# Performance work log

Hardware: AMD Instinct MI355X
Metric: run time of the kernel (lower is better)

## Reference

```python
import jax, jax.numpy as jnp
import numpy as np

CHN = 64
C8 = CHN // 8          # 8
ANG_IN = 5
ANG_OUT = 5
BU, V, H, W = 8, ANG_IN, 64, 64


def setup_inputs() -> dict:
    key = jax.random.key(0)
    ks = jax.random.split(key, 7)
    s = 0.05
    buffer = jax.random.normal(ks[0], (BU, CHN, V, H, W), jnp.float32)
    # 1x1x1 Conv3d weights stored as [out_ch, in_ch]
    Wq = jax.random.normal(ks[1], (C8, CHN), jnp.float32) * s
    Wk = jax.random.normal(ks[2], (C8, CHN), jnp.float32) * s
    Wv = jax.random.normal(ks[3], (C8 * ANG_OUT, CHN), jnp.float32) * s
    Wc = jax.random.normal(ks[4], (C8 * ANG_OUT, CHN), jnp.float32) * s
    # out block: Conv3d(40->64, k=(1,1,7), pad (0,0,3)); Conv3d(64->64, k=(7,1,1), pad (3,0,0))
    W1 = jax.random.normal(ks[5], (CHN, C8 * ANG_IN, 1, 1, 7), jnp.float32) * s
    W2 = jax.random.normal(ks[6], (CHN, CHN, 7, 1, 1), jnp.float32) * s
    return {"buffer": buffer, "Wq": Wq, "Wk": Wk, "Wv": Wv, "Wc": Wc, "W1": W1, "W2": W2}


def _pointwise(Wo, x):
    # 1x1x1 Conv3d == channel GEMM
    return jnp.einsum('oc,bcvhw->bovhw', Wo, x)


def reference(buffer, Wq, Wk, Wv, Wc, W1, W2):
    bu, c, v, h, w = buffer.shape
    q = _pointwise(Wq, buffer)      # [bu, c8, v, h, w]
    k = _pointwise(Wk, buffer)      # [bu, c8, v, h, w]
    val = _pointwise(Wv, buffer)    # [bu, c8*ar_out, v, h, w]

    def flat(x):  # 'bu c v h w -> bu c h (v w)'
        return x.transpose(0, 1, 3, 2, 4).reshape(bu, x.shape[1], h, v * w)

    qf, kf, vf = flat(q), flat(k), flat(val)
    attn = jax.nn.softmax(jnp.einsum('bchm,bchn->bhmn', qf, kf), axis=-1)  # [bu,h,vw,vw]
    out = jnp.einsum('bhmn,bchn->bchm', attn, vf)                          # [bu,c8*ar_out,h,vw]
    out = out.reshape(bu, -1, h, v, w).transpose(0, 1, 3, 2, 4)            # [bu,c8*ar_out,v,h,w]

    out = out + _pointwise(Wc, buffer)
    # 'bu (c ar_out) v h w -> bu (c v) ar_out h w'
    c8 = out.shape[1] // ANG_OUT
    out = out.reshape(bu, c8, ANG_OUT, v, h, w).transpose(0, 1, 3, 2, 4, 5)
    out = out.reshape(bu, c8 * v, ANG_OUT, h, w)

    dn = ('NCDHW', 'OIDHW', 'NCDHW')
    out = jax.nn.relu(jax.lax.conv_general_dilated(
        out, W1, (1, 1, 1), [(0, 0), (0, 0), (3, 3)], dimension_numbers=dn))
    out = jax.nn.relu(jax.lax.conv_general_dilated(
        out, W2, (1, 1, 1), [(3, 3), (0, 0), (0, 0)], dimension_numbers=dn))
    return out  # [bu, chn, ar_out, h, w]
```

## Files before the change

### kernel.cpp

```cpp
#include <hip/hip_runtime.h>
#include <math.h>


typedef __attribute__((ext_vector_type(8))) short bf16x8;
typedef __attribute__((ext_vector_type(4))) short bf16x4;
typedef __attribute__((ext_vector_type(4))) float fp32x4;
typedef __attribute__((ext_vector_type(8))) unsigned short u16x8;

#define OFF_WP      0
#define OFF_Z       29696
#define OFF_W1P_US  12288
#define OFF_W2P_US  30720
#define OFF_QFH_US  13166592
#define OFF_KFH_US  14477312
#define OFF_VTH_US  15788032
#define OFF_ZB16_US 23652352

__device__ inline unsigned short f2b(float f) {
    unsigned u = __builtin_bit_cast(unsigned, f);
    u = (u + 0x7fffu + ((u >> 16) & 1u)) >> 16;
    return (unsigned short)u;
}

#if __has_builtin(__builtin_amdgcn_mfma_f32_16x16x16bf16_1k)
#define MFMA16(a, b, c) __builtin_amdgcn_mfma_f32_16x16x16bf16_1k(a, b, c, 0, 0, 0)
#else
static __device__ inline fp32x4 mfma16_asm(bf16x4 a, bf16x4 b, fp32x4 c) {
    asm("v_mfma_f32_16x16x16_bf16 %0, %1, %2, %0" : "+v"(c) : "v"(a), "v"(b));
    return c;
}
#define MFMA16(a, b, c) mfma16_asm(a, b, c)
#endif

__global__ void prep_weights(const float* __restrict__ Wq, const float* __restrict__ Wk,
                             const float* __restrict__ Wv, const float* __restrict__ Wc,
                             const float* __restrict__ W1, const float* __restrict__ W2,
                             float* __restrict__ ws) {
    int e = blockIdx.x * 256 + threadIdx.x;
    unsigned short* us = (unsigned short*)ws;
    if (e < 6144) {
        int og = e / 1536, r = e % 1536;
        int c = r / 24, l = r % 24;
        int o = og * 24 + l;
        float v;
        if (o < 8)       v = Wq[o * 64 + c];
        else if (o < 16) v = Wk[(o - 8) * 64 + c];
        else if (o < 56) v = Wv[(o - 16) * 64 + c];
        else             v = Wc[(o - 56) * 64 + c];
        ws[OFF_WP + e] = v;
    } else if (e < 6144 + 18432) {
        int t = e - 6144;
        int j = t & 7, lane = (t >> 3) & 63, ks = (t >> 9) % 9, wid = t / 4608;
        int oc = wid * 16 + (lane & 15);
        int k = ks * 32 + (lane >> 4) * 8 + j;
        float v = 0.f;
        if (k < 280) { int kw = k / 40, ic = k % 40; v = W1[oc * 280 + ic * 7 + kw]; }
        us[OFF_W1P_US + t] = f2b(v);
    } else if (e < 6144 + 18432 + 28672) {
        int t = e - 6144 - 18432;
        int j = t & 7, lane = (t >> 3) & 63, kk = (t >> 9) & 1, kd = (t >> 10) % 7, wid = t / 7168;
        int oc = wid * 16 + (lane & 15);
        int ic = kk * 32 + (lane >> 4) * 8 + j;
        us[OFF_W2P_US + t] = f2b(W2[oc * 448 + ic * 7 + kd]);
    }
}

__global__ __launch_bounds__(256) void proj_kernel(const float* __restrict__ buf,
                                                   float* __restrict__ ws) {
    __shared__ alignas(16) float xs[64 * 64];
    int b = blockIdx.x;
    int h = b & 63;
    int v = (b >> 6) % 5;
    int bu = b / 320;
    int tid = threadIdx.x, wid = tid >> 6, w = tid & 63;

    const float* xbase = buf + ((bu * 64) * 5 + v) * 4096 + h * 64;
    for (int e = tid; e < 1024; e += 256) {
        int c = e >> 4, wq = e & 15;
        *(float4*)&xs[c * 64 + wq * 4] = *(const float4*)&xbase[c * 20480 + wq * 4];
    }
    __syncthreads();

    int og = __builtin_amdgcn_readfirstlane(wid);
    const float* wp = ws + OFF_WP + og * 1536;

    float acc[24];
    #pragma unroll
    for (int l = 0; l < 24; l++) acc[l] = 0.f;
    for (int c = 0; c < 64; c++) {
        float x = xs[c * 64 + w];
        const float* wr = wp + c * 24;
        #pragma unroll
        for (int l = 0; l < 24; l++) acc[l] += wr[l] * x;
    }

    int site = bu * 64 + h;
    int n = v * 64 + w;
    unsigned short* base = (unsigned short*)ws;
    unsigned short* qfh = base + OFF_QFH_US;
    unsigned short* kfh = base + OFF_KFH_US;
    unsigned short* vth = base + OFF_VTH_US;
    float* z = ws + OFF_Z;

    if (og == 0) {
        u16x8 qv, kv;
        #pragma unroll
        for (int l = 0; l < 8; l++) { qv[l] = f2b(acc[l]); kv[l] = f2b(acc[8 + l]); }
        *(u16x8*)&qfh[(site * 320 + n) * 8] = qv;
        *(u16x8*)&kfh[(site * 320 + n) * 8] = kv;
        #pragma unroll
        for (int l = 16; l < 24; l++) vth[(site * 48 + (l - 16)) * 320 + n] = f2b(acc[l]);
    } else if (og == 1) {
        #pragma unroll
        for (int l = 0; l < 24; l++) vth[(site * 48 + 8 + l) * 320 + n] = f2b(acc[l]);
    } else if (og == 2) {
        #pragma unroll
        for (int l = 0; l < 8; l++) vth[(site * 48 + 32 + l) * 320 + n] = f2b(acc[l]);
        #pragma unroll
        for (int l = 8; l < 24; l++) {
            int j2 = l - 8;
            int c8 = j2 / 5, ar = j2 % 5;
            z[((bu * 40 + c8 * 5 + v) * 5 + ar) * 4096 + h * 64 + w] = acc[l];
        }
    } else {
        #pragma unroll
        for (int l = 0; l < 24; l++) {
            int j2 = 16 + l;
            int c8 = j2 / 5, ar = j2 % 5;
            z[((bu * 40 + c8 * 5 + v) * 5 + ar) * 4096 + h * 64 + w] = acc[l];
        }
        #pragma unroll
        for (int j = 40; j < 48; j++)
            vth[(site * 48 + j) * 320 + n] = (j == 40) ? (unsigned short)0x3F80 : (unsigned short)0;
    }
}

__global__ __launch_bounds__(256, 2) void attn_kernel(float* __restrict__ ws) {
    __shared__ alignas(16) short vt[48 * 328];
    __shared__ alignas(16) short kl[320 * 8];

    int bid = blockIdx.x;
    int chunk = bid >> 9;
    int site = bid & 511;
    int bu = site >> 6, h = site & 63;
    int tid = threadIdx.x;
    int wid = tid >> 6, lane = tid & 63;
    int col = lane & 15, quad = lane >> 4;

    const unsigned short* base = (const unsigned short*)ws;
    const unsigned short* qfh = base + OFF_QFH_US + site * 320 * 8;
    const unsigned short* kfh = base + OFF_KFH_US + site * 320 * 8;
    const unsigned short* vsrc = base + OFF_VTH_US + site * 48 * 320;
    float* z = ws + OFF_Z;
    unsigned short* zb16 = (unsigned short*)ws + OFF_ZB16_US;

    for (int e = tid; e < 48 * 40; e += 256) {
        int row = e / 40, c8o = e % 40;
        *(u16x8*)&vt[row * 328 + c8o * 8] = *(const u16x8*)&vsrc[row * 320 + c8o * 8];
    }
    for (int e = tid; e < 320; e += 256)
        *(u16x8*)&kl[e * 8] = *(const u16x8*)&kfh[e * 8];
    __syncthreads();

    int off0[4], off1[4], off2[4];
    #pragma unroll
    for (int r = 0; r < 4; r++) {
        int j0 = quad * 4 + r, j1 = j0 + 16, j2 = j0 + 32;
        off0[r] = ((j0 / 5) * 25 + j0 % 5) * 4096;
        off1[r] = ((j1 / 5) * 25 + j1 % 5) * 4096;
        off2[r] = ((j2 / 5) * 25 + j2 % 5) * 4096;
    }

    int mt = chunk * 4 + wid;
    int m0 = mt * 16;

    int v_idx = m0 >> 6, w0 = m0 & 63;
    int sbase = (bu * 200 + v_idx * 5) * 4096 + h * 64 + w0 + col;
    float* zb = z + sbase;
    float zold0[4], zold1[4], zold2[4];
    #pragma unroll
    for (int r = 0; r < 4; r++) {
        zold0[r] = zb[off0[r]];
        zold1[r] = zb[off1[r]];
        zold2[r] = (quad < 2) ? zb[off2[r]] : 0.f;
    }

    bf16x8 qa = (bf16x8)0;
    if (quad == 0) qa = *(const bf16x8*)&qfh[(m0 + col) * 8];

    fp32x4 acc0 = {0.f, 0.f, 0.f, 0.f}, acc1 = acc0, acc2 = acc0;

    for (int cc = 0; cc < 4; cc++) {
        fp32x4 sT[5];
        #pragma unroll
        for (int u = 0; u < 5; u++) {
            int nt = cc * 5 + u;
            bf16x8 kb = *(const bf16x8*)&kl[(nt * 16 + col) * 8];
            sT[u] = __builtin_amdgcn_mfma_f32_16x16x32_bf16(
                kb, qa, (fp32x4){0.f, 0.f, 0.f, 0.f}, 0, 0, 0);
        }
        #pragma unroll
        for (int u = 0; u < 5; u++) {
            int nt = cc * 5 + u;
            bf16x4 pa;
            #pragma unroll
            for (int r = 0; r < 4; r++) pa[r] = (short)f2b(__expf(sT[u][r]));
            const short* vb = &vt[nt * 16 + quad * 4];
            acc0 = MFMA16(*(const bf16x4*)&vb[(col) * 328],      pa, acc0);
            acc1 = MFMA16(*(const bf16x4*)&vb[(16 + col) * 328], pa, acc1);
            acc2 = MFMA16(*(const bf16x4*)&vb[(32 + col) * 328], pa, acc2);
        }
    }

    float L = __shfl(acc2[0], 32 + col, 64);
    float inv = 1.f / L;

    unsigned short* zsb = zb16 + sbase;
    #pragma unroll
    for (int r = 0; r < 4; r++) {
        zsb[off0[r]] = f2b(zold0[r] + acc0[r] * inv);
        zsb[off1[r]] = f2b(zold1[r] + acc1[r] * inv);
        if (quad < 2) zsb[off2[r]] = f2b(zold2[r] + acc2[r] * inv);
    }
}

__global__ __launch_bounds__(256) void conv12_mfma(float* __restrict__ ws,
                                                   float* __restrict__ out) {
    __shared__ alignas(16) unsigned short ol[320 * 72];
    __shared__ alignas(16) unsigned short zl2[2][72 * 40];
    int b = blockIdx.x;
    int bu = b >> 6, h = b & 63;
    int tid = threadIdx.x, wid = tid >> 6, lane = tid & 63;
    int col = lane & 15, quad = lane >> 4;
    const unsigned short* zb16 = (const unsigned short*)ws + OFF_ZB16_US;

    const unsigned short* w1p = (const unsigned short*)ws + OFF_W1P_US;
    bf16x8 a1[9];
    #pragma unroll
    for (int ks = 0; ks < 9; ks++)
        a1[ks] = *(const bf16x8*)&w1p[((wid * 9 + ks) * 64 + lane) * 8];

    #define STAGE_AR(ar_, bufi_)                                                          \
        {                                                                                 \
            unsigned short* zb_ = zl2[bufi_];                                             \
            if (tid < 160) {                                                              \
                int wpi = tid / 20, icd = tid % 20;                                       \
                int wp = wpi < 3 ? wpi : wpi + 64;                                        \
                ((unsigned*)zb_)[wp * 20 + icd] = 0u;                                     \
            }                                                                             \
            for (int icq = wid; icq < 10; icq += 4) {                                     \
                const unsigned short* src = zb16 + ((bu * 40 + icq * 4) * 5 + (ar_)) * 4096 + h * 64 + lane; \
                ushort4 v4;                                                               \
                v4.x = src[0];                                                            \
                v4.y = src[20480];                                                        \
                v4.z = src[40960];                                                        \
                v4.w = src[61440];                                                        \
                *(ushort4*)&zb_[(3 + lane) * 40 + icq * 4] = v4;                          \
            }                                                                             \
        }

    STAGE_AR(0, 0);
    __syncthreads();
    for (int ar = 0; ar < 5; ar++) {
        if (ar < 4) STAGE_AR(ar + 1, (ar + 1) & 1);
        const unsigned short* zb = zl2[ar & 1];
        #pragma unroll
        for (int w4 = 0; w4 < 4; w4++) {
            int bb = (w4 * 16 + col) * 40;
            fp32x4 acc = {0.f, 0.f, 0.f, 0.f};
            #pragma unroll
            for (int ks = 0; ks < 9; ks++) {
                bf16x8 bf = *(const bf16x8*)&zb[bb + ks * 32 + quad * 8];
                acc = __builtin_amdgcn_mfma_f32_16x16x32_bf16(a1[ks], bf, acc, 0, 0, 0);
            }
            ushort4 o;
            o.x = f2b(fmaxf(acc[0], 0.f));
            o.y = f2b(fmaxf(acc[1], 0.f));
            o.z = f2b(fmaxf(acc[2], 0.f));
            o.w = f2b(fmaxf(acc[3], 0.f));
            *(ushort4*)&ol[(ar * 64 + w4 * 16 + col) * 72 + wid * 16 + quad * 4] = o;
        }
        __syncthreads();
    }
    #undef STAGE_AR

    const unsigned short* w2p = (const unsigned short*)ws + OFF_W2P_US;
    bf16x8 a2[7][2];
    #pragma unroll
    for (int kd = 0; kd < 7; kd++)
        #pragma unroll
        for (int kk = 0; kk < 2; kk++)
            a2[kd][kk] = *(const bf16x8*)&w2p[(((wid * 7 + kd) * 2 + kk) * 64 + lane) * 8];

    for (int nt = 0; nt < 20; nt++) {
        int ar = nt >> 2, wbase = (nt & 3) * 16;
        fp32x4 acc = {0.f, 0.f, 0.f, 0.f};
        #pragma unroll
        for (int kd = 0; kd < 7; kd++) {
            int arp = ar + kd - 3;
            if (arp >= 0 && arp < 5) {
                int sb = (arp * 64 + wbase + col) * 72;
                #pragma unroll
                for (int kk = 0; kk < 2; kk++) {
                    bf16x8 bf = *(const bf16x8*)&ol[sb + kk * 32 + quad * 8];
                    acc = __builtin_amdgcn_mfma_f32_16x16x32_bf16(a2[kd][kk], bf, acc, 0, 0, 0);
                }
            }
        }
        int w = wbase + col;
        #pragma unroll
        for (int r = 0; r < 4; r++) {
            int oc = wid * 16 + quad * 4 + r;
            out[((bu * 64 + oc) * 5 + ar) * 4096 + h * 64 + w] = fmaxf(acc[r], 0.f);
        }
    }
}

extern "C" void kernel_launch(void* const* d_in, const int* in_sizes, int n_in,
                              void* d_out, int out_size, void* d_ws, size_t ws_size,
                              hipStream_t stream) {
    const float* buf = (const float*)d_in[0];
    const float* Wq  = (const float*)d_in[1];
    const float* Wk  = (const float*)d_in[2];
    const float* Wv  = (const float*)d_in[3];
    const float* Wc  = (const float*)d_in[4];
    const float* W1  = (const float*)d_in[5];
    const float* W2  = (const float*)d_in[6];
    float* ws  = (float*)d_ws;
    float* out = (float*)d_out;

    prep_weights<<<208, 256, 0, stream>>>(Wq, Wk, Wv, Wc, W1, W2, ws);
    proj_kernel<<<2560, 256, 0, stream>>>(buf, ws);
    attn_kernel<<<2560, 256, 0, stream>>>(ws);
    conv12_mfma<<<512, 256, 0, stream>>>(ws, out);
}
```

Before: 163.0 us.

## Compute QKV/C projection with bf16 MFMA instead of scalar FP32 FMA loop

Replaces the scalar FP32 per-thread 64x24 channel GEMM in the projection kernel with 16x16x32 bf16 MFMA instructions. Weights are now pre-packed in bf16 in MFMA lane layout, and input activations are converted to bf16 from shared memory. The output scatter is remapped to the MFMA accumulator layout. This lowers the ALU cost of the projection at the price of bf16 rounding of inputs and weights, including for the Wc residual path that was previously full FP32.

```diff
diff --git a/kernel.cpp b/kernel.cpp
--- a/kernel.cpp
+++ b/kernel.cpp
@@ -7,14 +7,14 @@
 typedef __attribute__((ext_vector_type(4))) float fp32x4;
 typedef __attribute__((ext_vector_type(8))) unsigned short u16x8;
 
-#define OFF_WP      0
-#define OFF_Z       29696
+#define OFF_WPJ_US  0
 #define OFF_W1P_US  12288
 #define OFF_W2P_US  30720
 #define OFF_QFH_US  13166592
 #define OFF_KFH_US  14477312
 #define OFF_VTH_US  15788032
 #define OFF_ZB16_US 23652352
+#define OFF_Z       29696
 
 __device__ inline unsigned short f2b(float f) {
     unsigned u = __builtin_bit_cast(unsigned, f);
@@ -39,15 +39,15 @@
     int e = blockIdx.x * 256 + threadIdx.x;
     unsigned short* us = (unsigned short*)ws;
     if (e < 6144) {
-        int og = e / 1536, r = e % 1536;
-        int c = r / 24, l = r % 24;
-        int o = og * 24 + l;
+        int mt = e >> 10, kt = (e >> 9) & 1, lane = (e >> 3) & 63, j = e & 7;
+        int m = mt * 16 + (lane & 15);
+        int k = kt * 32 + ((lane >> 4) & 3) * 8 + j;
         float v;
-        if (o < 8)       v = Wq[o * 64 + c];
-        else if (o < 16) v = Wk[(o - 8) * 64 + c];
-        else if (o < 56) v = Wv[(o - 16) * 64 + c];
-        else             v = Wc[(o - 56) * 64 + c];
-        ws[OFF_WP + e] = v;
+        if (m < 8)       v = Wq[m * 64 + k];
+        else if (m < 16) v = Wk[(m - 8) * 64 + k];
+        else if (m < 56) v = Wv[(m - 16) * 64 + k];
+        else             v = Wc[(m - 56) * 64 + k];
+        us[OFF_WPJ_US + e] = f2b(v);
     } else if (e < 6144 + 18432) {
         int t = e - 6144;
         int j = t & 7, lane = (t >> 3) & 63, ks = (t >> 9) % 9, wid = t / 4608;
@@ -72,66 +72,88 @@
     int h = b & 63;
     int v = (b >> 6) % 5;
     int bu = b / 320;
-    int tid = threadIdx.x, wid = tid >> 6, w = tid & 63;
+    int tid = threadIdx.x, wid = tid >> 6, lane = tid & 63;
+    int col = lane & 15, quad = lane >> 4;
 
     const float* xbase = buf + ((bu * 64) * 5 + v) * 4096 + h * 64;
     for (int e = tid; e < 1024; e += 256) {
         int c = e >> 4, wq = e & 15;
         *(float4*)&xs[c * 64 + wq * 4] = *(const float4*)&xbase[c * 20480 + wq * 4];
     }
+
+    const unsigned short* wpj = (const unsigned short*)ws + OFF_WPJ_US;
+    bf16x8 aw[6][2];
+    #pragma unroll
+    for (int mt = 0; mt < 6; mt++)
+        #pragma unroll
+        for (int kt = 0; kt < 2; kt++)
+            aw[mt][kt] = *(const bf16x8*)&wpj[((mt * 2 + kt) * 64 + lane) * 8];
+
     __syncthreads();
 
-    int og = __builtin_amdgcn_readfirstlane(wid);
-    const float* wp = ws + OFF_WP + og * 1536;
-
-    float acc[24];
-    #pragma unroll
-    for (int l = 0; l < 24; l++) acc[l] = 0.f;
-    for (int c = 0; c < 64; c++) {
-        float x = xs[c * 64 + w];
-        const float* wr = wp + c * 24;
-        #pragma unroll
-        for (int l = 0; l < 24; l++) acc[l] += wr[l] * x;
-    }
+    int n0 = wid * 16;
+    bf16x8 xb[2];
+    #pragma unroll
+    for (int kt = 0; kt < 2; kt++) {
+        u16x8 t;
+        #pragma unroll
+        for (int j = 0; j < 8; j++)
+            t[j] = f2b(xs[(kt * 32 + quad * 8 + j) * 64 + n0 + col]);
+        xb[kt] = __builtin_bit_cast(bf16x8, t);
+    }
+
+    fp32x4 acc[6];
+    #pragma unroll
+    for (int mt = 0; mt < 6; mt++) acc[mt] = (fp32x4){0.f, 0.f, 0.f, 0.f};
+    #pragma unroll
+    for (int kt = 0; kt < 2; kt++)
+        #pragma unroll
+        for (int mt = 0; mt < 6; mt++)
+            acc[mt] = __builtin_amdgcn_mfma_f32_16x16x32_bf16(aw[mt][kt], xb[kt], acc[mt], 0, 0, 0);
 
     int site = bu * 64 + h;
-    int n = v * 64 + w;
+    int w = n0 + col;
+    int n_flat = v * 64 + w;
     unsigned short* base = (unsigned short*)ws;
     unsigned short* qfh = base + OFF_QFH_US;
     unsigned short* kfh = base + OFF_KFH_US;
     unsigned short* vth = base + OFF_VTH_US;
     float* z = ws + OFF_Z;
 
-    if (og == 0) {
-        u16x8 qv, kv;
-        #pragma unroll
-        for (int l = 0; l < 8; l++) { qv[l] = f2b(acc[l]); kv[l] = f2b(acc[8 + l]); }
-        *(u16x8*)&qfh[(site * 320 + n) * 8] = qv;
-        *(u16x8*)&kfh[(site * 320 + n) * 8] = kv;
-        #pragma unroll
-        for (int l = 16; l < 24; l++) vth[(site * 48 + (l - 16)) * 320 + n] = f2b(acc[l]);
-    } else if (og == 1) {
-        #pragma unroll
-        for (int l = 0; l < 24; l++) vth[(site * 48 + 8 + l) * 320 + n] = f2b(acc[l]);
-    } else if (og == 2) {
-        #pragma unroll
-        for (int l = 0; l < 8; l++) vth[(site * 48 + 32 + l) * 320 + n] = f2b(acc[l]);
-        #pragma unroll
-        for (int l = 8; l < 24; l++) {
-            int j2 = l - 8;
-            int c8 = j2 / 5, ar = j2 % 5;
-            z[((bu * 40 + c8 * 5 + v) * 5 + ar) * 4096 + h * 64 + w] = acc[l];
-        }
+    {
+        ushort4 o;
+        o.x = f2b(acc[0][0]); o.y = f2b(acc[0][1]); o.z = f2b(acc[0][2]); o.w = f2b(acc[0][3]);
+        if (quad < 2) *(ushort4*)&qfh[(site * 320 + n_flat) * 8 + quad * 4] = o;
+        else          *(ushort4*)&kfh[(site * 320 + n_flat) * 8 + (quad - 2) * 4] = o;
+    }
+    #pragma unroll
+    for (int r = 0; r < 4; r++) {
+        vth[(site * 48 + quad * 4 + r) * 320 + n_flat]      = f2b(acc[1][r]);
+        vth[(site * 48 + 16 + quad * 4 + r) * 320 + n_flat] = f2b(acc[2][r]);
+    }
+    if (quad < 2) {
+        #pragma unroll
+        for (int r = 0; r < 4; r++)
+            vth[(site * 48 + 32 + quad * 4 + r) * 320 + n_flat] = f2b(acc[3][r]);
     } else {
         #pragma unroll
-        for (int l = 0; l < 24; l++) {
-            int j2 = 16 + l;
-            int c8 = j2 / 5, ar = j2 % 5;
-            z[((bu * 40 + c8 * 5 + v) * 5 + ar) * 4096 + h * 64 + w] = acc[l];
-        }
+        for (int r = 0; r < 4; r++) {
+            int jc = (quad - 2) * 4 + r;
+            z[((bu * 40 + (jc / 5) * 5 + v) * 5 + (jc % 5)) * 4096 + h * 64 + w] = acc[3][r];
+        }
+    }
+    #pragma unroll
+    for (int r = 0; r < 4; r++) {
+        int jc4 = 8 + quad * 4 + r;
+        z[((bu * 40 + (jc4 / 5) * 5 + v) * 5 + (jc4 % 5)) * 4096 + h * 64 + w] = acc[4][r];
+        int jc5 = 24 + quad * 4 + r;
+        z[((bu * 40 + (jc5 / 5) * 5 + v) * 5 + (jc5 % 5)) * 4096 + h * 64 + w] = acc[5][r];
+    }
+    if (wid == 3) {
         #pragma unroll
         for (int j = 40; j < 48; j++)
-            vth[(site * 48 + j) * 320 + n] = (j == 40) ? (unsigned short)0x3F80 : (unsigned short)0;
+            vth[(site * 48 + j) * 320 + v * 64 + lane] =
+                (j == 40) ? (unsigned short)0x3F80 : (unsigned short)0;
     }
 }
 
```

Result: faster. 155.9 us (-4.3%).
